# Optimization experiments

Hardware: AMD Instinct MI355X
Metric: run time of the kernel (lower is better)

Reference implementation:

```python
import jax, jax.numpy as jnp
import numpy as np

B, D, K = 32, 400, 200
H = 8            # kernel_size (GRU hidden)
LAYERS = 4
OUT = 8


def setup_inputs() -> dict:
    key = jax.random.key(0)
    ks = jax.random.split(key, 16)
    x = jax.random.normal(ks[0], (B, D, K), dtype=jnp.float32)
    # variable-length zero padding along time per (b, k) sequence
    lengths = jax.random.randint(ks[1], (B, K), D // 2, D + 1)
    tmask = jnp.arange(D)[None, :, None] < lengths[:, None, :]   # (B, D, K)
    x = x * tmask
    s = 1.0 / np.sqrt(H)
    def u(k, shape):
        return jax.random.uniform(k, shape, jnp.float32, -s, s)
    return {
        "x": x,
        "w_ih0": u(ks[2], (2, 3 * H, 1)),
        "w_hh0": u(ks[3], (2, 3 * H, H)),
        "b_ih0": u(ks[4], (2, 3 * H)),
        "b_hh0": u(ks[5], (2, 3 * H)),
        "w_ih": u(ks[6], (LAYERS - 1, 2, 3 * H, 2 * H)),
        "w_hh": u(ks[7], (LAYERS - 1, 2, 3 * H, H)),
        "b_ih": u(ks[8], (LAYERS - 1, 2, 3 * H)),
        "b_hh": u(ks[9], (LAYERS - 1, 2, 3 * H)),
        "lin1_w": u(ks[10], (H, 2 * H)),
        "lin1_b": u(ks[11], (H,)),
        "lin2_w": u(ks[12], (OUT, H)),
        "lin2_b": u(ks[13], (OUT,)),
    }


def _gru_dir(x, mask, Wih, Whh, bih, bhh):
    # x: (N, T, in), mask: (N, T) bool -> (N, T, H); zero past each length
    gi = jnp.einsum('nti,gi->tng', x, Wih) + bih          # (T, N, 3H) input gates
    m = mask.T[:, :, None]                                 # (T, N, 1)
    h0 = jnp.zeros((x.shape[0], Whh.shape[1]), x.dtype)
    def step(h, inp):
        gi_t, m_t = inp
        gh = h @ Whh.T + bhh
        ir, iz, inn = jnp.split(gi_t, 3, axis=-1)          # PyTorch gate order r, z, n
        hr, hz, hn = jnp.split(gh, 3, axis=-1)
        r = jax.nn.sigmoid(ir + hr)
        z = jax.nn.sigmoid(iz + hz)
        n = jnp.tanh(inn + r * hn)
        h = jnp.where(m_t, (1.0 - z) * n + z * h, h)
        return h, jnp.where(m_t, h, 0.0)
    _, out = jax.lax.scan(step, h0, (gi, m))
    return out.transpose(1, 0, 2)


def _bidir_gru(x, mask, rev_idx, p):
    Wih, Whh, bih, bhh = p
    fwd = _gru_dir(x, mask, Wih[0], Whh[0], bih[0], bhh[0])
    # backward dir of a packed sequence: reverse within each valid region
    x_rev = jnp.take_along_axis(x, rev_idx[:, :, None], axis=1)
    bwd_rev = _gru_dir(x_rev, mask, Wih[1], Whh[1], bih[1], bhh[1])
    bwd = jnp.take_along_axis(bwd_rev, rev_idx[:, :, None], axis=1)
    bwd = jnp.where(mask[:, :, None], bwd, 0.0)
    return jnp.concatenate([fwd, bwd], axis=-1)


def _forward(x, w_ih0, w_hh0, b_ih0, b_hh0, w_ih, w_hh, b_ih, b_hh,
             lin1_w, lin1_b, lin2_w, lin2_b):
    b, d, k = x.shape
    seq = x.transpose(0, 2, 1).reshape(b * k, d, 1)         # (N, T, 1)
    vals = seq[:, :, 0]
    zm = vals == 0.0
    lengths = jnp.where(zm.any(axis=1), jnp.argmax(zm, axis=1), d)  # (N,)
    mask = jnp.arange(d)[None, :] < lengths[:, None]        # (N, T)
    rev_idx = jnp.clip(lengths[:, None] - 1 - jnp.arange(d)[None, :], 0, d - 1)
    h = _bidir_gru(seq, mask, rev_idx, (w_ih0, w_hh0, b_ih0, b_hh0))
    for l in range(w_ih.shape[0]):                          # layers 1..3
        h = _bidir_gru(h, mask, rev_idx, (w_ih[l], w_hh[l], b_ih[l], b_hh[l]))
    # last valid timestep per sequence (matches argmax-of-all-zero gather)
    last = jnp.take_along_axis(h, (lengths - 1)[:, None, None], axis=1)[:, 0, :]
    feat = last.reshape(b, k, -1)                           # (B, K, 2H)
    y = jax.nn.leaky_relu(feat @ lin1_w.T + lin1_b, negative_slope=0.2)
    return y @ lin2_w.T + lin2_b                            # (B, K, OUT)


def reference(x, w_ih0, w_hh0, b_ih0, b_hh0, w_ih, w_hh, b_ih, b_hh,
              lin1_w, lin1_b, lin2_w, lin2_b):
    return _forward(x, w_ih0, w_hh0, b_ih0, b_hh0, w_ih, w_hh, b_ih, b_hh,
                    lin1_w, lin1_b, lin2_w, lin2_b)
```

## Files before the change

kernel.cpp:

```cpp
#include <hip/hip_runtime.h>

#define BB 32
#define DD 400
#define KK 200
#define NN (BB*KK)
#define NBINS 512
#define NSIMD 1024

typedef float f2 __attribute__((ext_vector_type(2)));
typedef _Float16 half_t;
typedef _Float16 f16x2 __attribute__((ext_vector_type(2)));

#if defined(__has_builtin)
#if __has_builtin(__builtin_amdgcn_fdot2)
#define HAVE_FDOT2 1
#endif
#endif

__device__ __forceinline__ float dot2(f16x2 w, f16x2 v, float acc) {
#ifdef HAVE_FDOT2
  return __builtin_amdgcn_fdot2(w, v, acc, false);
#else
  return fmaf((float)w.x, (float)v.x, fmaf((float)w.y, (float)v.y, acc));
#endif
}

__device__ __forceinline__ float fast_sigmoid(float x) {
  float e = __builtin_amdgcn_exp2f(-1.4426950408889634f * x);
  return __builtin_amdgcn_rcpf(1.0f + e);
}
__device__ __forceinline__ float fast_tanh(float x) {
  float e = __builtin_amdgcn_exp2f(-2.8853900817779268f * x);
  return 2.0f * __builtin_amdgcn_rcpf(1.0f + e) - 1.0f;
}

#define QPERM(v, P) __int_as_float(__builtin_amdgcn_mov_dpp(__float_as_int(v), (P)*0x55, 0xF, 0xF, true))
#define HMIRROR(v) __int_as_float(__builtin_amdgcn_mov_dpp(__float_as_int(v), 0x141, 0xF, 0xF, true))

__global__ __launch_bounds__(256) void transpose_x(const float* __restrict__ x,
                                                   float* __restrict__ xt) {
  __shared__ float tile[32][33];
  int b = blockIdx.x, t0 = blockIdx.y * 32, k0 = blockIdx.z * 32;
  int tx = threadIdx.x, ty = threadIdx.y;
#pragma unroll
  for (int i = 0; i < 32; i += 8) {
    int t = t0 + ty + i, k = k0 + tx;
    tile[ty + i][tx] = (t < DD && k < KK) ? x[((size_t)b * DD + t) * KK + k] : 0.0f;
  }
  __syncthreads();
#pragma unroll
  for (int i = 0; i < 32; i += 8) {
    int k = k0 + ty + i, t = t0 + tx;
    if (k < KK && t < DD) xt[((size_t)b * KK + k) * DD + t] = tile[tx][ty + i];
  }
}

__global__ __launch_bounds__(64) void compute_lengths(const float* __restrict__ xt,
                                                      int* __restrict__ lengths,
                                                      int* __restrict__ hist) {
  int n = blockIdx.x, lane = threadIdx.x;
  int m = DD;
  for (int t = lane; t < DD; t += 64) {
    if (xt[(size_t)n * DD + t] == 0.0f) { m = t; break; }
  }
#pragma unroll
  for (int off = 1; off < 64; off <<= 1) {
    int o = __shfl_xor(m, off, 64);
    m = (o < m) ? o : m;
  }
  if (lane == 0) {
    lengths[n] = m;
    atomicAdd(&hist[m], 1);
  }
}

__global__ __launch_bounds__(64) void scan_offsets(const int* __restrict__ hist,
                                                   int* __restrict__ offs) {
  int lane = threadIdx.x;
  int v[8], tot = 0;
#pragma unroll
  for (int i = 0; i < 8; ++i) { v[i] = tot; tot += hist[lane * 8 + i]; }
  int incl = tot;
#pragma unroll
  for (int off = 1; off < 64; off <<= 1) {
    int oth = __shfl_up(incl, off, 64);
    if (lane >= off) incl += oth;
  }
  int excl = incl - tot;
#pragma unroll
  for (int i = 0; i < 8; ++i) offs[lane * 8 + i] = excl + v[i];
}

__global__ __launch_bounds__(256) void scatter_sort(const int* __restrict__ lengths,
                                                    int* __restrict__ offs,
                                                    int* __restrict__ order,
                                                    int* __restrict__ len_sorted) {
  int n = blockIdx.x * 256 + threadIdx.x;
  if (n >= NN) return;
  int len = lengths[n];
  int pos = atomicAdd(&offs[len], 1);
  order[pos] = n;
  len_sorted[pos] = len;
}

__device__ __forceinline__ int octet_of_wave(int p, int W) {
  int E = W - NSIMD;
  if (E <= 0) return W - 1 - p;
  if (p >= NSIMD) return p - NSIMD;
  if (p >= E) return W - 1 - (p - E);
  return (W - 1 - NSIMD + E) - p;
}

template <int IN_DIM, bool IND_IN, bool WRITE_SEQ, bool FWD_ONLY>
__global__ __launch_bounds__(64) void gru_scan(
    const void* __restrict__ in, half_t* __restrict__ out, float* __restrict__ feat,
    const int* __restrict__ len_sorted, const int* __restrict__ order,
    const float* __restrict__ Wih, const float* __restrict__ Whh,
    const float* __restrict__ bih, const float* __restrict__ bhh, int nseq) {
  int p = blockIdx.x;
  int lane = threadIdx.x & 63;
  int G = FWD_ONLY ? nseq : nseq * 2;
  int W = (G + 7) >> 3;
  if (p >= W) return;
  int o = octet_of_wave(p, W);
  int gidx = o * 8 + (lane >> 3);
  int li = lane & 7;
  if (gidx >= G) return;
  int sg  = FWD_ONLY ? gidx : (gidx >> 1);
  int dir = FWD_ONLY ? 0 : (gidx & 1);
  int len = len_sorted[sg];

  int qb = li & 4;
  f2 wAB[3][4];
  f16x2 wi2[3][8];
  float wi1[3];
  float bs[3], bh2;
#pragma unroll
  for (int gt = 0; gt < 3; ++gt) {
    int row = dir * 24 + gt * 8 + li;
    if constexpr (IN_DIM == 16) {
#pragma unroll
      for (int q = 0; q < 8; ++q) {
        f16x2 w;
        w.x = (half_t)Wih[row * 16 + 2 * q];
        w.y = (half_t)Wih[row * 16 + 2 * q + 1];
        wi2[gt][q] = w;
      }
    } else {
      wi1[gt] = Wih[row];
    }
#pragma unroll
    for (int P = 0; P < 4; ++P) {
      f2 w;
      w.x = Whh[row * 8 + qb + P];
      w.y = Whh[row * 8 + ((qb + P) ^ 7)];
      wAB[gt][P] = w;
    }
    bs[gt] = bih[row] + ((gt < 2) ? bhh[row] : 0.0f);
    if (gt == 2) bh2 = bhh[row];
  }

  int steps = len;
  float h = 0.0f;

  const float* px = nullptr;
  const half_t* pxh = nullptr;
  ptrdiff_t xstep;
  if constexpr (IN_DIM == 1) {
    const float* basep = (const float*)in + (IND_IN ? (size_t)order[sg] * DD : (size_t)sg * DD);
    px = basep + ((dir == 0) ? 0 : (len - 1));
    xstep = (dir == 0) ? 1 : -1;
  } else {
    const half_t* basep = (const half_t*)in + (size_t)sg * DD * 16;
    pxh = basep + (size_t)((dir == 0) ? 0 : (len - 1)) * 16;
    xstep = (dir == 0) ? 16 : -16;
  }

  half_t* pw = nullptr; ptrdiff_t wstep = 0;
  if constexpr (WRITE_SEQ) {
    pw = out + ((size_t)sg * DD + ((dir == 0) ? 0 : (len - 1))) * 16 + dir * 8 + li;
    wstep = (dir == 0) ? 16 : -16;
  }

  auto core = [&](float a0, float a1, float a2) {
    float hm = HMIRROR(h);
    float hq0 = QPERM(h, 0), hq1 = QPERM(h, 1), hq2 = QPERM(h, 2), hq3 = QPERM(h, 3);
    float hx0 = QPERM(hm, 0), hx1 = QPERM(hm, 1), hx2 = QPERM(hm, 2), hx3 = QPERM(hm, 3);
    f2 u0; u0.x = hq0; u0.y = hx0;
    f2 u1; u1.x = hq1; u1.y = hx1;
    f2 u2; u2.x = hq2; u2.y = hx2;
    f2 u3; u3.x = hq3; u3.y = hx3;

    f2 c0a = wAB[0][0] * u0; c0a += wAB[0][1] * u1;
    f2 c0b = wAB[0][2] * u2; c0b += wAB[0][3] * u3;
    f2 c0 = c0a + c0b;
    f2 c1a = wAB[1][0] * u0; c1a += wAB[1][1] * u1;
    f2 c1b = wAB[1][2] * u2; c1b += wAB[1][3] * u3;
    f2 c1 = c1a + c1b;
    f2 c2a = wAB[2][0] * u0; c2a += wAB[2][1] * u1;
    f2 c2b = wAB[2][2] * u2; c2b += wAB[2][3] * u3;
    f2 c2 = c2a + c2b;

    float r = fast_sigmoid(a0 + c0.x + c0.y);
    float z = fast_sigmoid(a1 + c1.x + c1.y);
    float n = fast_tanh(a2 + r * (bh2 + c2.x + c2.y));
    h = z * (h - n) + n;
    if constexpr (WRITE_SEQ) { *pw = (half_t)h; pw += wstep; }
  };

  if constexpr (IN_DIM == 1) {
    float s0_, s1_, s2_, s3_;
    auto ld = [&](float& S_) { S_ = *px; px += xstep; };
    auto st = [&](float& S_, bool pf) {
      float a0 = fmaf(wi1[0], S_, bs[0]);
      float a1 = fmaf(wi1[1], S_, bs[1]);
      float a2 = fmaf(wi1[2], S_, bs[2]);
      if (pf) ld(S_);
      core(a0, a1, a2);
    };
    ld(s0_); ld(s1_); ld(s2_); ld(s3_);
    int t = 0;
    for (; t + 4 <= steps; t += 4) {
      st(s0_, true); st(s1_, true); st(s2_, true); st(s3_, true);
    }
    int rem = steps - t;
    if (rem > 0) st(s0_, false);
    if (rem > 1) st(s1_, false);
    if (rem > 2) st(s2_, false);
  } else {
    uint4 b0_[2], b1_[2], b2_[2], b3_[2];
    auto ld = [&](uint4 (&B_)[2]) {
      const uint4* q4 = reinterpret_cast<const uint4*>(pxh);
      B_[0] = q4[0]; B_[1] = q4[1];
      pxh += xstep;
    };
    auto st = [&](uint4 (&B_)[2], bool pf) {
      float a0 = bs[0], a1 = bs[1], a2 = bs[2];
#pragma unroll
      for (int q = 0; q < 2; ++q) {
        f16x2 p0 = __builtin_bit_cast(f16x2, B_[q].x);
        f16x2 p1 = __builtin_bit_cast(f16x2, B_[q].y);
        f16x2 p2 = __builtin_bit_cast(f16x2, B_[q].z);
        f16x2 p3 = __builtin_bit_cast(f16x2, B_[q].w);
        a0 = dot2(wi2[0][4*q], p0, a0); a0 = dot2(wi2[0][4*q+1], p1, a0);
        a0 = dot2(wi2[0][4*q+2], p2, a0); a0 = dot2(wi2[0][4*q+3], p3, a0);
        a1 = dot2(wi2[1][4*q], p0, a1); a1 = dot2(wi2[1][4*q+1], p1, a1);
        a1 = dot2(wi2[1][4*q+2], p2, a1); a1 = dot2(wi2[1][4*q+3], p3, a1);
        a2 = dot2(wi2[2][4*q], p0, a2); a2 = dot2(wi2[2][4*q+1], p1, a2);
        a2 = dot2(wi2[2][4*q+2], p2, a2); a2 = dot2(wi2[2][4*q+3], p3, a2);
      }
      if (pf) ld(B_);
      core(a0, a1, a2);
    };
    ld(b0_); ld(b1_); ld(b2_); ld(b3_);
    int t = 0;
    for (; t + 4 <= steps; t += 4) {
      st(b0_, true); st(b1_, true); st(b2_, true); st(b3_, true);
    }
    int rem = steps - t;
    if (rem > 0) st(b0_, false);
    if (rem > 1) st(b1_, false);
    if (rem > 2) st(b2_, false);
  }

  if constexpr (!WRITE_SEQ) {
    feat[(size_t)order[sg] * 16 + dir * 8 + li] = h;
  }
}

__global__ __launch_bounds__(256) void bwd_last(
    const half_t* __restrict__ in, float* __restrict__ feat,
    const int* __restrict__ len_sorted, const int* __restrict__ order,
    const float* __restrict__ Wih, const float* __restrict__ bih,
    const float* __restrict__ bhh, int nseq) {
  int tid = blockIdx.x * blockDim.x + threadIdx.x;
  int sg = tid >> 3, li = tid & 7;
  if (sg >= nseq) return;
  int len = len_sorted[sg];
  const half_t* xp = in + ((size_t)sg * DD + (len - 1)) * 16;
  float xv[16];
#pragma unroll
  for (int j = 0; j < 16; ++j) xv[j] = (float)xp[j];
  float a[3], bh[3];
#pragma unroll
  for (int gt = 0; gt < 3; ++gt) {
    int row = 24 + gt * 8 + li;
    const float* wp = Wih + row * 16;
    float acc = bih[row];
#pragma unroll
    for (int j = 0; j < 16; ++j) acc = fmaf(wp[j], xv[j], acc);
    a[gt] = acc;
    bh[gt] = bhh[row];
  }
  float r = fast_sigmoid(a[0] + bh[0]);
  float z = fast_sigmoid(a[1] + bh[1]);
  float n = fast_tanh(a[2] + r * bh[2]);
  float h = (1.0f - z) * n;
  feat[(size_t)order[sg] * 16 + 8 + li] = h;
}

__global__ __launch_bounds__(256) void head_kernel(
    const float* __restrict__ feat, const float* __restrict__ w1,
    const float* __restrict__ b1, const float* __restrict__ w2,
    const float* __restrict__ b2, float* __restrict__ out) {
  int n = blockIdx.x * blockDim.x + threadIdx.x;
  if (n >= NN) return;
  float f[16];
  const float4* p = reinterpret_cast<const float4*>(feat + (size_t)n * 16);
#pragma unroll
  for (int q = 0; q < 4; ++q) {
    float4 v = p[q];
    f[4*q] = v.x; f[4*q+1] = v.y; f[4*q+2] = v.z; f[4*q+3] = v.w;
  }
  float y[8];
#pragma unroll
  for (int o = 0; o < 8; ++o) {
    float s = b1[o];
#pragma unroll
    for (int j = 0; j < 16; ++j) s += f[j] * w1[o * 16 + j];
    y[o] = (s > 0.0f) ? s : 0.2f * s;
  }
#pragma unroll
  for (int o2 = 0; o2 < 8; ++o2) {
    float s = b2[o2];
#pragma unroll
    for (int o = 0; o < 8; ++o) s += y[o] * w2[o2 * 8 + o];
    out[(size_t)n * 8 + o2] = s;
  }
}

extern "C" void kernel_launch(void* const* d_in, const int* in_sizes, int n_in,
                              void* d_out, int out_size, void* d_ws, size_t ws_size,
                              hipStream_t stream) {
  const float* x      = (const float*)d_in[0];
  const float* w_ih0  = (const float*)d_in[1];
  const float* w_hh0  = (const float*)d_in[2];
  const float* b_ih0  = (const float*)d_in[3];
  const float* b_hh0  = (const float*)d_in[4];
  const float* w_ih   = (const float*)d_in[5];
  const float* w_hh   = (const float*)d_in[6];
  const float* b_ih   = (const float*)d_in[7];
  const float* b_hh   = (const float*)d_in[8];
  const float* lin1_w = (const float*)d_in[9];
  const float* lin1_b = (const float*)d_in[10];
  const float* lin2_w = (const float*)d_in[11];
  const float* lin2_b = (const float*)d_in[12];
  float* out = (float*)d_out;

  char* ws = (char*)d_ws;
  size_t off = 0;
  auto alloc = [&](size_t bytes) -> void* {
    void* p = ws + off;
    off += (bytes + 255) & ~(size_t)255;
    return p;
  };
  alloc(1024);
  float* xt         = (float*)alloc((size_t)NN * DD * sizeof(float) + 1024);
  int*   lengths    = (int*)  alloc((size_t)NN * sizeof(int));
  int*   hist       = (int*)  alloc(NBINS * sizeof(int));
  int*   offs       = (int*)  alloc(NBINS * sizeof(int));
  int*   order      = (int*)  alloc((size_t)NN * sizeof(int));
  int*   len_sorted = (int*)  alloc((size_t)NN * sizeof(int));
  float* feat       = (float*)alloc((size_t)NN * 16 * sizeof(float));
  size_t base = off;
  size_t per_seq = (size_t)DD * 16 * sizeof(half_t) * 2 + 1024;
  int Nc = NN;
  if (base + (size_t)NN * per_seq + 8192 > ws_size) {
    size_t avail = (ws_size > base + 8192) ? (ws_size - base - 8192) : 0;
    size_t nc = avail / per_seq;
    if (nc < 1) nc = 1;
    if (nc > (size_t)NN) nc = NN;
    Nc = (int)nc;
  }
  alloc(1024);
  half_t* bufA = (half_t*)alloc((size_t)Nc * DD * 16 * sizeof(half_t) + 1024);
  half_t* bufB = (half_t*)alloc((size_t)Nc * DD * 16 * sizeof(half_t) + 1024);

  hipMemsetAsync(hist, 0, NBINS * sizeof(int), stream);
  dim3 gT(BB, (DD + 31) / 32, (KK + 31) / 32), bT(32, 8, 1);
  hipLaunchKernelGGL(transpose_x, gT, bT, 0, stream, x, xt);
  hipLaunchKernelGGL(compute_lengths, dim3(NN), dim3(64), 0, stream, xt, lengths, hist);
  hipLaunchKernelGGL(scan_offsets, dim3(1), dim3(64), 0, stream, hist, offs);
  hipLaunchKernelGGL(scatter_sort, dim3((NN + 255) / 256), dim3(256), 0, stream,
                     lengths, offs, order, len_sorted);

  for (int s0 = 0; s0 < NN; s0 += Nc) {
    int ns = (NN - s0 < Nc) ? (NN - s0) : Nc;
    int W2 = (ns * 2 + 7) / 8;
    int W1 = (ns + 7) / 8;
    int blk1 = (ns * 8 + 255) / 256;
    gru_scan<1, true, true, false><<<W2, 64, 0, stream>>>(
        (const void*)xt, bufA, nullptr, len_sorted + s0, order + s0,
        w_ih0, w_hh0, b_ih0, b_hh0, ns);
    gru_scan<16, false, true, false><<<W2, 64, 0, stream>>>(
        (const void*)bufA, bufB, nullptr, len_sorted + s0, order + s0,
        w_ih + 0 * 2 * 24 * 16, w_hh + 0 * 2 * 24 * 8,
        b_ih + 0 * 2 * 24, b_hh + 0 * 2 * 24, ns);
    gru_scan<16, false, true, false><<<W2, 64, 0, stream>>>(
        (const void*)bufB, bufA, nullptr, len_sorted + s0, order + s0,
        w_ih + 1 * 2 * 24 * 16, w_hh + 1 * 2 * 24 * 8,
        b_ih + 1 * 2 * 24, b_hh + 1 * 2 * 24, ns);
    gru_scan<16, false, false, true><<<W1, 64, 0, stream>>>(
        (const void*)bufA, nullptr, feat, len_sorted + s0, order + s0,
        w_ih + 2 * 2 * 24 * 16, w_hh + 2 * 2 * 24 * 8,
        b_ih + 2 * 2 * 24, b_hh + 2 * 2 * 24, ns);
    hipLaunchKernelGGL(bwd_last, dim3(blk1), dim3(256), 0, stream,
                       bufA, feat, len_sorted + s0, order + s0,
                       w_ih + 2 * 2 * 24 * 16, b_ih + 2 * 2 * 24, b_hh + 2 * 2 * 24, ns);
  }
  hipLaunchKernelGGL(head_kernel, dim3((NN + 255) / 256), dim3(256), 0, stream,
                     feat, lin1_w, lin1_b, lin2_w, lin2_b, out);
}
```

Measured before the change: 414.8 us.

## Run forward and backward GRU directions in the same wave with octet-interleaved layout

Each wave now processes 8 sequences and runs both directions interleaved, so the independent forward and backward recurrences can hide each other's latency within one instruction stream. Intermediate buffers move to a slab layout of 8 sequences per timestep (128 halfs), which makes each timestep's writes and reads contiguous across the wave. The SIMD-aware wave-to-octet mapping is replaced by simple reverse ordering, and the chunk size is rounded to a multiple of 8. The cost is half as many waves, which lowers parallelism, and roughly double the register use per thread.

```diff
diff --git a/kernel.cpp b/kernel.cpp
--- a/kernel.cpp
+++ b/kernel.cpp
@@ -5,24 +5,13 @@
 #define KK 200
 #define NN (BB*KK)
 #define NBINS 512
-#define NSIMD 1024
 
 typedef float f2 __attribute__((ext_vector_type(2)));
 typedef _Float16 half_t;
 typedef _Float16 f16x2 __attribute__((ext_vector_type(2)));
 
-#if defined(__has_builtin)
-#if __has_builtin(__builtin_amdgcn_fdot2)
-#define HAVE_FDOT2 1
-#endif
-#endif
-
 __device__ __forceinline__ float dot2(f16x2 w, f16x2 v, float acc) {
-#ifdef HAVE_FDOT2
   return __builtin_amdgcn_fdot2(w, v, acc, false);
-#else
-  return fmaf((float)w.x, (float)v.x, fmaf((float)w.y, (float)v.y, acc));
-#endif
 }
 
 __device__ __forceinline__ float fast_sigmoid(float x) {
@@ -103,86 +92,72 @@
   len_sorted[pos] = len;
 }
 
-__device__ __forceinline__ int octet_of_wave(int p, int W) {
-  int E = W - NSIMD;
-  if (E <= 0) return W - 1 - p;
-  if (p >= NSIMD) return p - NSIMD;
-  if (p >= E) return W - 1 - (p - E);
-  return (W - 1 - NSIMD + E) - p;
-}
-
-template <int IN_DIM, bool IND_IN, bool WRITE_SEQ, bool FWD_ONLY>
-__global__ __launch_bounds__(64) void gru_scan(
-    const void* __restrict__ in, half_t* __restrict__ out, float* __restrict__ feat,
+template <int IN_DIM>
+__global__ __launch_bounds__(64) void gru_bidir(
+    const void* __restrict__ in, half_t* __restrict__ out,
     const int* __restrict__ len_sorted, const int* __restrict__ order,
     const float* __restrict__ Wih, const float* __restrict__ Whh,
     const float* __restrict__ bih, const float* __restrict__ bhh, int nseq) {
+  int W = nseq >> 3;
   int p = blockIdx.x;
+  if (p >= W) return;
+  int o = W - 1 - p;
   int lane = threadIdx.x & 63;
-  int G = FWD_ONLY ? nseq : nseq * 2;
-  int W = (G + 7) >> 3;
-  if (p >= W) return;
-  int o = octet_of_wave(p, W);
-  int gidx = o * 8 + (lane >> 3);
-  int li = lane & 7;
-  if (gidx >= G) return;
-  int sg  = FWD_ONLY ? gidx : (gidx >> 1);
-  int dir = FWD_ONLY ? 0 : (gidx & 1);
+  int s8 = lane >> 3, li = lane & 7;
+  int sg = o * 8 + s8;
   int len = len_sorted[sg];
-
   int qb = li & 4;
-  f2 wAB[3][4];
-  f16x2 wi2[3][8];
-  float wi1[3];
-  float bs[3], bh2;
+
+  f2 wABf[3][4], wABb[3][4];
+  f16x2 wif[3][8], wib[3][8];
+  float w1f[3], w1b[3];
+  float bsf[3], bsb[3], bh2f, bh2b;
 #pragma unroll
   for (int gt = 0; gt < 3; ++gt) {
-    int row = dir * 24 + gt * 8 + li;
+    int rf = gt * 8 + li, rb = 24 + gt * 8 + li;
     if constexpr (IN_DIM == 16) {
 #pragma unroll
       for (int q = 0; q < 8; ++q) {
-        f16x2 w;
-        w.x = (half_t)Wih[row * 16 + 2 * q];
-        w.y = (half_t)Wih[row * 16 + 2 * q + 1];
-        wi2[gt][q] = w;
+        f16x2 a; a.x = (half_t)Wih[rf * 16 + 2*q]; a.y = (half_t)Wih[rf * 16 + 2*q + 1];
+        wif[gt][q] = a;
+        f16x2 b; b.x = (half_t)Wih[rb * 16 + 2*q]; b.y = (half_t)Wih[rb * 16 + 2*q + 1];
+        wib[gt][q] = b;
       }
     } else {
-      wi1[gt] = Wih[row];
+      w1f[gt] = Wih[rf];
+      w1b[gt] = Wih[rb];
     }
 #pragma unroll
     for (int P = 0; P < 4; ++P) {
-      f2 w;
-      w.x = Whh[row * 8 + qb + P];
-      w.y = Whh[row * 8 + ((qb + P) ^ 7)];
-      wAB[gt][P] = w;
-    }
-    bs[gt] = bih[row] + ((gt < 2) ? bhh[row] : 0.0f);
-    if (gt == 2) bh2 = bhh[row];
-  }
-
-  int steps = len;
-  float h = 0.0f;
-
-  const float* px = nullptr;
-  const half_t* pxh = nullptr;
-  ptrdiff_t xstep;
+      f2 a; a.x = Whh[rf * 8 + qb + P]; a.y = Whh[rf * 8 + ((qb + P) ^ 7)];
+      wABf[gt][P] = a;
+      f2 b; b.x = Whh[rb * 8 + qb + P]; b.y = Whh[rb * 8 + ((qb + P) ^ 7)];
+      wABb[gt][P] = b;
+    }
+    bsf[gt] = bih[rf] + ((gt < 2) ? bhh[rf] : 0.0f);
+    bsb[gt] = bih[rb] + ((gt < 2) ? bhh[rb] : 0.0f);
+    if (gt == 2) { bh2f = bhh[rf]; bh2b = bhh[rb]; }
+  }
+
+  float hf = 0.0f, hb = 0.0f;
+
+  const float* pxf1 = nullptr; const float* pxb1 = nullptr;
+  const half_t* pxf = nullptr; const half_t* pxb = nullptr;
   if constexpr (IN_DIM == 1) {
-    const float* basep = (const float*)in + (IND_IN ? (size_t)order[sg] * DD : (size_t)sg * DD);
-    px = basep + ((dir == 0) ? 0 : (len - 1));
-    xstep = (dir == 0) ? 1 : -1;
+    const float* base = (const float*)in + (size_t)order[sg] * DD;
+    pxf1 = base;
+    pxb1 = base + (len - 1);
   } else {
-    const half_t* basep = (const half_t*)in + (size_t)sg * DD * 16;
-    pxh = basep + (size_t)((dir == 0) ? 0 : (len - 1)) * 16;
-    xstep = (dir == 0) ? 16 : -16;
-  }
-
-  half_t* pw = nullptr; ptrdiff_t wstep = 0;
-  if constexpr (WRITE_SEQ) {
-    pw = out + ((size_t)sg * DD + ((dir == 0) ? 0 : (len - 1))) * 16 + dir * 8 + li;
-    wstep = (dir == 0) ? 16 : -16;
-  }
-
-  auto core = [&](float a0, float a1, float a2) {
+    const half_t* slab = (const half_t*)in + (size_t)o * DD * 128;
+    pxf = slab + s8 * 8;
+    pxb = slab + (size_t)(len - 1) * 128 + s8 * 8;
+  }
+  half_t* ob  = out + (size_t)o * DD * 128;
+  half_t* pwf = ob + lane;
+  half_t* pwb = ob + (size_t)(len - 1) * 128 + 64 + lane;
+
+  auto core1 = [&](float& h, f2 (&wAB)[3][4], float bh2v,
+                   float a0, float a1, float a2, half_t*& pw, ptrdiff_t ws) {
     float hm = HMIRROR(h);
     float hq0 = QPERM(h, 0), hq1 = QPERM(h, 1), hq2 = QPERM(h, 2), hq3 = QPERM(h, 3);
     float hx0 = QPERM(hm, 0), hx1 = QPERM(hm, 1), hx2 = QPERM(hm, 2), hx3 = QPERM(hm, 3);
@@ -190,7 +165,6 @@
     f2 u1; u1.x = hq1; u1.y = hx1;
     f2 u2; u2.x = hq2; u2.y = hx2;
     f2 u3; u3.x = hq3; u3.y = hx3;
-
     f2 c0a = wAB[0][0] * u0; c0a += wAB[0][1] * u1;
     f2 c0b = wAB[0][2] * u2; c0b += wAB[0][3] * u3;
     f2 c0 = c0a + c0b;
@@ -200,72 +174,179 @@
     f2 c2a = wAB[2][0] * u0; c2a += wAB[2][1] * u1;
     f2 c2b = wAB[2][2] * u2; c2b += wAB[2][3] * u3;
     f2 c2 = c2a + c2b;
-
     float r = fast_sigmoid(a0 + c0.x + c0.y);
     float z = fast_sigmoid(a1 + c1.x + c1.y);
-    float n = fast_tanh(a2 + r * (bh2 + c2.x + c2.y));
+    float n = fast_tanh(a2 + r * (bh2v + c2.x + c2.y));
     h = z * (h - n) + n;
-    if constexpr (WRITE_SEQ) { *pw = (half_t)h; pw += wstep; }
+    *pw = (half_t)h; pw += ws;
   };
 
   if constexpr (IN_DIM == 1) {
-    float s0_, s1_, s2_, s3_;
-    auto ld = [&](float& S_) { S_ = *px; px += xstep; };
-    auto st = [&](float& S_, bool pf) {
-      float a0 = fmaf(wi1[0], S_, bs[0]);
-      float a1 = fmaf(wi1[1], S_, bs[1]);
-      float a2 = fmaf(wi1[2], S_, bs[2]);
-      if (pf) ld(S_);
-      core(a0, a1, a2);
+    float ff0, ff1, ff2, ff3, bb0, bb1, bb2, bb3;
+    auto ld = [&](float& F_, float& B_) { F_ = *pxf1++; B_ = *pxb1--; };
+    auto st = [&](float& F_, float& B_, bool pf) {
+      float a0f = fmaf(w1f[0], F_, bsf[0]);
+      float a1f = fmaf(w1f[1], F_, bsf[1]);
+      float a2f = fmaf(w1f[2], F_, bsf[2]);
+      float a0b = fmaf(w1b[0], B_, bsb[0]);
+      float a1b = fmaf(w1b[1], B_, bsb[1]);
+      float a2b = fmaf(w1b[2], B_, bsb[2]);
+      if (pf) ld(F_, B_);
+      core1(hf, wABf, bh2f, a0f, a1f, a2f, pwf, 128);
+      core1(hb, wABb, bh2b, a0b, a1b, a2b, pwb, -128);
     };
-    ld(s0_); ld(s1_); ld(s2_); ld(s3_);
+    ld(ff0, bb0); ld(ff1, bb1); ld(ff2, bb2); ld(ff3, bb3);
     int t = 0;
-    for (; t + 4 <= steps; t += 4) {
-      st(s0_, true); st(s1_, true); st(s2_, true); st(s3_, true);
-    }
-    int rem = steps - t;
-    if (rem > 0) st(s0_, false);
-    if (rem > 1) st(s1_, false);
-    if (rem > 2) st(s2_, false);
+    for (; t + 4 <= len; t += 4) {
+      st(ff0, bb0, true); st(ff1, bb1, true); st(ff2, bb2, true); st(ff3, bb3, true);
+    }
+    int rem = len - t;
+    if (rem > 0) st(ff0, bb0, false);
+    if (rem > 1) st(ff1, bb1, false);
+    if (rem > 2) st(ff2, bb2, false);
   } else {
-    uint4 b0_[2], b1_[2], b2_[2], b3_[2];
-    auto ld = [&](uint4 (&B_)[2]) {
-      const uint4* q4 = reinterpret_cast<const uint4*>(pxh);
-      B_[0] = q4[0]; B_[1] = q4[1];
-      pxh += xstep;
+    uint4 F0[2], F1[2], F2[2], F3[2], B0[2], B1[2], B2[2], B3[2];
+    auto ld = [&](uint4 (&F_)[2], uint4 (&B_)[2]) {
+      const uint4* qf = reinterpret_cast<const uint4*>(pxf);
+      F_[0] = qf[0]; F_[1] = qf[8];
+      pxf += 128;
+      const uint4* qbp = reinterpret_cast<const uint4*>(pxb);
+      B_[0] = qbp[0]; B_[1] = qbp[8];
+      pxb -= 128;
     };
-    auto st = [&](uint4 (&B_)[2], bool pf) {
-      float a0 = bs[0], a1 = bs[1], a2 = bs[2];
+    auto gi3 = [&](uint4 (&X_)[2], f16x2 (&wi)[3][8], const float* bsv,
+                   float& a0, float& a1, float& a2) {
+      a0 = bsv[0]; a1 = bsv[1]; a2 = bsv[2];
 #pragma unroll
       for (int q = 0; q < 2; ++q) {
-        f16x2 p0 = __builtin_bit_cast(f16x2, B_[q].x);
-        f16x2 p1 = __builtin_bit_cast(f16x2, B_[q].y);
-        f16x2 p2 = __builtin_bit_cast(f16x2, B_[q].z);
-        f16x2 p3 = __builtin_bit_cast(f16x2, B_[q].w);
-        a0 = dot2(wi2[0][4*q], p0, a0); a0 = dot2(wi2[0][4*q+1], p1, a0);
-        a0 = dot2(wi2[0][4*q+2], p2, a0); a0 = dot2(wi2[0][4*q+3], p3, a0);
-        a1 = dot2(wi2[1][4*q], p0, a1); a1 = dot2(wi2[1][4*q+1], p1, a1);
-        a1 = dot2(wi2[1][4*q+2], p2, a1); a1 = dot2(wi2[1][4*q+3], p3, a1);
-        a2 = dot2(wi2[2][4*q], p0, a2); a2 = dot2(wi2[2][4*q+1], p1, a2);
-        a2 = dot2(wi2[2][4*q+2], p2, a2); a2 = dot2(wi2[2][4*q+3], p3, a2);
+        f16x2 p0 = __builtin_bit_cast(f16x2, X_[q].x);
+        f16x2 p1 = __builtin_bit_cast(f16x2, X_[q].y);
+        f16x2 p2 = __builtin_bit_cast(f16x2, X_[q].z);
+        f16x2 p3 = __builtin_bit_cast(f16x2, X_[q].w);
+        a0 = dot2(wi[0][4*q], p0, a0); a0 = dot2(wi[0][4*q+1], p1, a0);
+        a0 = dot2(wi[0][4*q+2], p2, a0); a0 = dot2(wi[0][4*q+3], p3, a0);
+        a1 = dot2(wi[1][4*q], p0, a1); a1 = dot2(wi[1][4*q+1], p1, a1);
+        a1 = dot2(wi[1][4*q+2], p2, a1); a1 = dot2(wi[1][4*q+3], p3, a1);
+        a2 = dot2(wi[2][4*q], p0, a2); a2 = dot2(wi[2][4*q+1], p1, a2);
+        a2 = dot2(wi[2][4*q+2], p2, a2); a2 = dot2(wi[2][4*q+3], p3, a2);
       }
-      if (pf) ld(B_);
-      core(a0, a1, a2);
     };
-    ld(b0_); ld(b1_); ld(b2_); ld(b3_);
+    auto st = [&](uint4 (&F_)[2], uint4 (&B_)[2], bool pf) {
+      float a0f, a1f, a2f, a0b, a1b, a2b;
+      gi3(F_, wif, bsf, a0f, a1f, a2f);
+      gi3(B_, wib, bsb, a0b, a1b, a2b);
+      if (pf) ld(F_, B_);
+      core1(hf, wABf, bh2f, a0f, a1f, a2f, pwf, 128);
+      core1(hb, wABb, bh2b, a0b, a1b, a2b, pwb, -128);
+    };
+    ld(F0, B0); ld(F1, B1); ld(F2, B2); ld(F3, B3);
     int t = 0;
-    for (; t + 4 <= steps; t += 4) {
-      st(b0_, true); st(b1_, true); st(b2_, true); st(b3_, true);
-    }
-    int rem = steps - t;
-    if (rem > 0) st(b0_, false);
-    if (rem > 1) st(b1_, false);
-    if (rem > 2) st(b2_, false);
-  }
-
-  if constexpr (!WRITE_SEQ) {
-    feat[(size_t)order[sg] * 16 + dir * 8 + li] = h;
-  }
+    for (; t + 4 <= len; t += 4) {
+      st(F0, B0, true); st(F1, B1, true); st(F2, B2, true); st(F3, B3, true);
+    }
+    int rem = len - t;
+    if (rem > 0) st(F0, B0, false);
+    if (rem > 1) st(F1, B1, false);
+    if (rem > 2) st(F2, B2, false);
+  }
+}
+
+__global__ __launch_bounds__(64) void gru_fwd_last(
+    const half_t* __restrict__ in, float* __restrict__ feat,
+    const int* __restrict__ len_sorted, const int* __restrict__ order,
+    const float* __restrict__ Wih, const float* __restrict__ Whh,
+    const float* __restrict__ bih, const float* __restrict__ bhh, int nseq) {
+  int W = nseq >> 3;
+  int p = blockIdx.x;
+  if (p >= W) return;
+  int o = W - 1 - p;
+  int lane = threadIdx.x & 63;
+  int s8 = lane >> 3, li = lane & 7;
+  int sg = o * 8 + s8;
+  int len = len_sorted[sg];
+  int qb = li & 4;
+
+  f2 wAB[3][4];
+  f16x2 wi2[3][8];
+  float bs[3], bh2v;
+#pragma unroll
+  for (int gt = 0; gt < 3; ++gt) {
+    int row = gt * 8 + li;
+#pragma unroll
+    for (int q = 0; q < 8; ++q) {
+      f16x2 w; w.x = (half_t)Wih[row * 16 + 2*q]; w.y = (half_t)Wih[row * 16 + 2*q + 1];
+      wi2[gt][q] = w;
+    }
+#pragma unroll
+    for (int P = 0; P < 4; ++P) {
+      f2 w; w.x = Whh[row * 8 + qb + P]; w.y = Whh[row * 8 + ((qb + P) ^ 7)];
+      wAB[gt][P] = w;
+    }
+    bs[gt] = bih[row] + ((gt < 2) ? bhh[row] : 0.0f);
+    if (gt == 2) bh2v = bhh[row];
+  }
+
+  float h = 0.0f;
+  const half_t* pxf = in + (size_t)o * DD * 128 + s8 * 8;
+
+  auto core1 = [&](float a0, float a1, float a2) {
+    float hm = HMIRROR(h);
+    float hq0 = QPERM(h, 0), hq1 = QPERM(h, 1), hq2 = QPERM(h, 2), hq3 = QPERM(h, 3);
+    float hx0 = QPERM(hm, 0), hx1 = QPERM(hm, 1), hx2 = QPERM(hm, 2), hx3 = QPERM(hm, 3);
+    f2 u0; u0.x = hq0; u0.y = hx0;
+    f2 u1; u1.x = hq1; u1.y = hx1;
+    f2 u2; u2.x = hq2; u2.y = hx2;
+    f2 u3; u3.x = hq3; u3.y = hx3;
+    f2 c0a = wAB[0][0] * u0; c0a += wAB[0][1] * u1;
+    f2 c0b = wAB[0][2] * u2; c0b += wAB[0][3] * u3;
+    f2 c0 = c0a + c0b;
+    f2 c1a = wAB[1][0] * u0; c1a += wAB[1][1] * u1;
+    f2 c1b = wAB[1][2] * u2; c1b += wAB[1][3] * u3;
+    f2 c1 = c1a + c1b;
+    f2 c2a = wAB[2][0] * u0; c2a += wAB[2][1] * u1;
+    f2 c2b = wAB[2][2] * u2; c2b += wAB[2][3] * u3;
+    f2 c2 = c2a + c2b;
+    float r = fast_sigmoid(a0 + c0.x + c0.y);
+    float z = fast_sigmoid(a1 + c1.x + c1.y);
+    float n = fast_tanh(a2 + r * (bh2v + c2.x + c2.y));
+    h = z * (h - n) + n;
+  };
+
+  uint4 F0[2], F1[2], F2[2], F3[2];
+  auto ld = [&](uint4 (&F_)[2]) {
+    const uint4* q = reinterpret_cast<const uint4*>(pxf);
+    F_[0] = q[0]; F_[1] = q[8];
+    pxf += 128;
+  };
+  auto st = [&](uint4 (&F_)[2], bool pf) {
+    float a0 = bs[0], a1 = bs[1], a2 = bs[2];
+#pragma unroll
+    for (int q = 0; q < 2; ++q) {
+      f16x2 p0 = __builtin_bit_cast(f16x2, F_[q].x);
+      f16x2 p1 = __builtin_bit_cast(f16x2, F_[q].y);
+      f16x2 p2 = __builtin_bit_cast(f16x2, F_[q].z);
+      f16x2 p3 = __builtin_bit_cast(f16x2, F_[q].w);
+      a0 = dot2(wi2[0][4*q], p0, a0); a0 = dot2(wi2[0][4*q+1], p1, a0);
+      a0 = dot2(wi2[0][4*q+2], p2, a0); a0 = dot2(wi2[0][4*q+3], p3, a0);
+      a1 = dot2(wi2[1][4*q], p0, a1); a1 = dot2(wi2[1][4*q+1], p1, a1);
+      a1 = dot2(wi2[1][4*q+2], p2, a1); a1 = dot2(wi2[1][4*q+3], p3, a1);
+      a2 = dot2(wi2[2][4*q], p0, a2); a2 = dot2(wi2[2][4*q+1], p1, a2);
+      a2 = dot2(wi2[2][4*q+2], p2, a2); a2 = dot2(wi2[2][4*q+3], p3, a2);
+    }
+    if (pf) ld(F_);
+    core1(a0, a1, a2);
+  };
+  ld(F0); ld(F1); ld(F2); ld(F3);
+  int t = 0;
+  for (; t + 4 <= len; t += 4) {
+    st(F0, true); st(F1, true); st(F2, true); st(F3, true);
+  }
+  int rem = len - t;
+  if (rem > 0) st(F0, false);
+  if (rem > 1) st(F1, false);
+  if (rem > 2) st(F2, false);
+
+  feat[(size_t)order[sg] * 16 + li] = h;
 }
 
 __global__ __launch_bounds__(256) void bwd_last(
@@ -277,10 +358,11 @@
   int sg = tid >> 3, li = tid & 7;
   if (sg >= nseq) return;
   int len = len_sorted[sg];
-  const half_t* xp = in + ((size_t)sg * DD + (len - 1)) * 16;
+  int o = sg >> 3;
+  const half_t* xp = in + ((size_t)o * DD + (len - 1)) * 128 + (sg & 7) * 8;
   float xv[16];
 #pragma unroll
-  for (int j = 0; j < 16; ++j) xv[j] = (float)xp[j];
+  for (int j = 0; j < 8; ++j) { xv[j] = (float)xp[j]; xv[8 + j] = (float)xp[64 + j]; }
   float a[3], bh[3];
 #pragma unroll
   for (int gt = 0; gt < 3; ++gt) {
@@ -354,8 +436,8 @@
     off += (bytes + 255) & ~(size_t)255;
     return p;
   };
-  alloc(1024);
-  float* xt         = (float*)alloc((size_t)NN * DD * sizeof(float) + 1024);
+  alloc(2048);
+  float* xt         = (float*)alloc((size_t)NN * DD * sizeof(float) + 2048);
   int*   lengths    = (int*)  alloc((size_t)NN * sizeof(int));
   int*   hist       = (int*)  alloc(NBINS * sizeof(int));
   int*   offs       = (int*)  alloc(NBINS * sizeof(int));
@@ -365,16 +447,16 @@
   size_t base = off;
   size_t per_seq = (size_t)DD * 16 * sizeof(half_t) * 2 + 1024;
   int Nc = NN;
-  if (base + (size_t)NN * per_seq + 8192 > ws_size) {
-    size_t avail = (ws_size > base + 8192) ? (ws_size - base - 8192) : 0;
+  if (base + (size_t)NN * per_seq + 16384 > ws_size) {
+    size_t avail = (ws_size > base + 16384) ? (ws_size - base - 16384) : 0;
     size_t nc = avail / per_seq;
-    if (nc < 1) nc = 1;
+    if (nc < 8) nc = 8;
     if (nc > (size_t)NN) nc = NN;
-    Nc = (int)nc;
-  }
-  alloc(1024);
-  half_t* bufA = (half_t*)alloc((size_t)Nc * DD * 16 * sizeof(half_t) + 1024);
-  half_t* bufB = (half_t*)alloc((size_t)Nc * DD * 16 * sizeof(half_t) + 1024);
+    Nc = (int)(nc & ~(size_t)7);
+  }
+  alloc(2048);
+  half_t* bufA = (half_t*)alloc((size_t)Nc * DD * 16 * sizeof(half_t) + 2048);
+  half_t* bufB = (half_t*)alloc((size_t)Nc * DD * 16 * sizeof(half_t) + 2048);
 
   hipMemsetAsync(hist, 0, NBINS * sizeof(int), stream);
   dim3 gT(BB, (DD + 31) / 32, (KK + 31) / 32), bT(32, 8, 1);
@@ -386,22 +468,21 @@
 
   for (int s0 = 0; s0 < NN; s0 += Nc) {
     int ns = (NN - s0 < Nc) ? (NN - s0) : Nc;
-    int W2 = (ns * 2 + 7) / 8;
-    int W1 = (ns + 7) / 8;
+    int Wb = ns / 8;
     int blk1 = (ns * 8 + 255) / 256;
-    gru_scan<1, true, true, false><<<W2, 64, 0, stream>>>(
-        (const void*)xt, bufA, nullptr, len_sorted + s0, order + s0,
+    gru_bidir<1><<<Wb, 64, 0, stream>>>(
+        (const void*)xt, bufA, len_sorted + s0, order + s0,
         w_ih0, w_hh0, b_ih0, b_hh0, ns);
-    gru_scan<16, false, true, false><<<W2, 64, 0, stream>>>(
-        (const void*)bufA, bufB, nullptr, len_sorted + s0, order + s0,
+    gru_bidir<16><<<Wb, 64, 0, stream>>>(
+        (const void*)bufA, bufB, len_sorted + s0, order + s0,
         w_ih + 0 * 2 * 24 * 16, w_hh + 0 * 2 * 24 * 8,
         b_ih + 0 * 2 * 24, b_hh + 0 * 2 * 24, ns);
-    gru_scan<16, false, true, false><<<W2, 64, 0, stream>>>(
-        (const void*)bufB, bufA, nullptr, len_sorted + s0, order + s0,
+    gru_bidir<16><<<Wb, 64, 0, stream>>>(
+        (const void*)bufB, bufA, len_sorted + s0, order + s0,
         w_ih + 1 * 2 * 24 * 16, w_hh + 1 * 2 * 24 * 8,
         b_ih + 1 * 2 * 24, b_hh + 1 * 2 * 24, ns);
-    gru_scan<16, false, false, true><<<W1, 64, 0, stream>>>(
-        (const void*)bufA, nullptr, feat, len_sorted + s0, order + s0,
+    hipLaunchKernelGGL(gru_fwd_last, dim3(Wb), dim3(64), 0, stream,
+        bufA, feat, len_sorted + s0, order + s0,
         w_ih + 2 * 2 * 24 * 16, w_hh + 2 * 2 * 24 * 8,
         b_ih + 2 * 2 * 24, b_hh + 2 * 2 * 24, ns);
     hipLaunchKernelGGL(bwd_last, dim3(blk1), dim3(256), 0, stream,
```

Result: slower. 522.0 us (+25.9%).
